# Performance work log

Hardware: AMD Instinct MI355X
Metric: run time of the kernel (lower is better)

The kernel has to match this reference:

```python
import jax, jax.numpy as jnp
import numpy as np

EPS = 1e-5

def _bn(x, g, b):
    # training-mode batchnorm over all axes except the last (channel)
    axes = tuple(range(x.ndim - 1))
    m = x.mean(axis=axes, keepdims=True)
    v = x.var(axis=axes, keepdims=True)
    return (x - m) * jax.lax.rsqrt(v + EPS) * g + b

def setup_inputs() -> dict:
    key = jax.random.key(0)
    ks = jax.random.split(key, 9)
    B, N = 4, 4096
    def w(i, shape, fan_in):
        return jax.random.normal(ks[i], shape, jnp.float32) * np.float32(1.0 / np.sqrt(fan_in))
    return {
        "x": jax.random.normal(ks[0], (B, 3, N), jnp.float32),
        "Wq": w(1, (64, 3), 3),
        "Wkv": w(2, (128, 3), 3),
        "Wp1": w(3, (64, 3), 3),
        "Wp2": w(4, (64, 64), 64),
        "Wa": w(5, (64, 64), 64),
        "Wc1": w(6, (64, 64), 64),
        "Wsk": w(7, (64, 6), 6),
        "Wga": w(8, (64, 128), 128),
        "g_p": jnp.ones(64, jnp.float32), "b_p": jnp.zeros(64, jnp.float32),
        "g_a": jnp.ones(64, jnp.float32), "b_a": jnp.zeros(64, jnp.float32),
        "g_c": jnp.ones(64, jnp.float32), "b_c": jnp.zeros(64, jnp.float32),
        "g_sk": jnp.ones(64, jnp.float32), "b_sk": jnp.zeros(64, jnp.float32),
        "g_ga": jnp.ones(64, jnp.float32), "b_ga": jnp.zeros(64, jnp.float32),
        "k": 32,
    }

def reference(x, Wq, Wkv, Wp1, Wp2, Wa, Wc1, Wsk, Wga,
              g_p, b_p, g_a, b_a, g_c, b_c, g_sk, b_sk, g_ga, b_ga, k):
    # x: [B, 3, N] point cloud
    xt = jnp.transpose(x, (0, 2, 1))                      # [B, N, 3]
    B = xt.shape[0]
    # --- KNN neighbor grouping (irregular gather) ---
    sq = jnp.sum(xt * xt, axis=-1)                        # [B, N]
    dist = sq[:, :, None] + sq[:, None, :] - 2.0 * jnp.einsum('bnc,bmc->bnm', xt, xt)
    _, idx = jax.lax.top_k(-dist, k)                      # [B, N, k]
    grouped = xt[jnp.arange(B)[:, None, None], idx]       # [B, N, k, 3]
    rel = grouped - xt[:, :, None, :]                     # relative coords
    # --- local self-attention (1x1 conv QKV + position encoding) ---
    q = jnp.einsum('bnc,dc->bnd', xt, Wq)[:, :, None, :]  # [B, N, 1, 64]
    kv = jnp.einsum('bnkc,dc->bnkd', rel, Wkv)            # [B, N, k, 128]
    kf, vf = kv[..., :64], kv[..., 64:]
    pos = jnp.einsum('bnkd,ed->bnke',
                     jax.nn.relu(_bn(jnp.einsum('bnkc,dc->bnkd', rel, Wp1), g_p, b_p)),
                     Wp2)                                 # [B, N, k, 64]
    logits = jax.nn.relu(_bn(jnp.einsum('bnkd,ed->bnke', q - kf + pos, Wa), g_a, b_a))
    attn = jax.nn.softmax(logits, axis=2)                 # softmax over k neighbors
    agg = jnp.sum(attn * (vf + pos), axis=2)              # [B, N, 64]
    # --- pointnet conv-BN head + skip + fusion ---
    h = jax.nn.relu(_bn(jnp.einsum('bnd,ed->bne', agg, Wc1), g_c, b_c))
    nb_max = jnp.max(grouped, axis=2)                     # [B, N, 3] max-pool over neighbors
    sk = jax.nn.relu(_bn(jnp.einsum('bnc,dc->bnd',
                                    jnp.concatenate([xt, nb_max], axis=-1), Wsk), g_sk, b_sk))
    out = jax.nn.relu(_bn(jnp.einsum('bnc,dc->bnd',
                                     jnp.concatenate([h, sk], axis=-1), Wga), g_ga, b_ga))
    return jnp.transpose(out, (0, 2, 1))                  # [B, 64, N]
```

## Files before the change

### kernel.cpp

```cpp
#include <hip/hip_runtime.h>

#define NBATCH 4
#define NPTS   4096
#define NP     (NBATCH*NPTS)
#define KK     32
#define INF    __builtin_inff()

static const size_t OFF_PTS  = 0;
static const size_t OFF_IDX  = 65536;
static const size_t OFF_TSK  = 589824;
static const size_t OFF_TC   = 1638400;
static const size_t OFF_TGA  = 2686976;
static const size_t OFF_PREL = 3735552;
static const size_t OFF_PSK  = 3735568;
static const size_t OFF_PTA  = 3735696;
static const size_t OFF_PTC  = 3735824;
static const size_t OFF_PTGA = 3735952;
static const size_t OFF_AFF  = 3736080;

typedef __bf16 bf16x8  __attribute__((ext_vector_type(8)));
typedef float  floatx16 __attribute__((ext_vector_type(16)));
#define MFMA32(a,b,c) __builtin_amdgcn_mfma_f32_32x32x16_bf16(a, b, c, 0, 0, 0)

union F8 { bf16x8 v; unsigned short us[8]; uint4 q4; };

__device__ __forceinline__ unsigned short bfbits(float f) {
  unsigned u = __float_as_uint(f);
  return (unsigned short)((u + 0x7FFFu + ((u >> 16) & 1u)) >> 16);
}
__device__ __forceinline__ floatx16 zero16() {
  floatx16 v;
#pragma unroll
  for (int i = 0; i < 16; ++i) v[i] = 0.f;
  return v;
}
__device__ __forceinline__ float wsum(float v) {
#pragma unroll
  for (int o = 32; o; o >>= 1) v += __shfl_xor(v, o, 64);
  return v;
}

__global__ __launch_bounds__(256,1) void k_prep(const float* __restrict__ x, float4* __restrict__ pts,
                                                float* __restrict__ pta, float* __restrict__ ptc,
                                                float* __restrict__ ptga, float* __restrict__ prel9,
                                                float* __restrict__ psk128) {
  if (blockIdx.x == 0) {
    if (threadIdx.x < 128) {
      pta[threadIdx.x] = 0.f; ptc[threadIdx.x] = 0.f; ptga[threadIdx.x] = 0.f;
      psk128[threadIdx.x] = 0.f;
    }
    if (threadIdx.x < 16) prel9[threadIdx.x] = 0.f;
  }
  int g = blockIdx.x * 256 + threadIdx.x;
  int b = g / NPTS, n = g % NPTS;
  float vx = x[(b*3+0)*NPTS + n];
  float vy = x[(b*3+1)*NPTS + n];
  float vz = x[(b*3+2)*NPTS + n];
  pts[g] = make_float4(vx, vy, vz, vx*vx + vy*vy + vz*vz);
}

__global__ __launch_bounds__(256) void k_knn(const float4* __restrict__ pts, int* __restrict__ idx,
                                             const float* __restrict__ Wsk, float* __restrict__ tsk,
                                             float* __restrict__ prel9, float* __restrict__ psk128) {
  __shared__ __align__(16) float4 tile[1024];
  __shared__ int ocnt[4];
  __shared__ int lsel[128];
  __shared__ float rsum[9], psum[64], pss[64];
  const int tid  = threadIdx.x;
  const int w    = tid >> 6;
  const int lane = tid & 63;
  if (tid < 9)  rsum[tid] = 0.f;
  if (tid < 64) { psum[tid] = 0.f; pss[tid] = 0.f; }
  const int n = blockIdx.x * 4 + w;
  const int batch = n >> 12;
  const float4* base = pts + batch * NPTS;
  const float4 me = pts[n];
  const float wk0 = Wsk[lane*6+0], wk1 = Wsk[lane*6+1], wk2 = Wsk[lane*6+2],
              wk3 = Wsk[lane*6+3], wk4 = Wsk[lane*6+4], wk5 = Wsk[lane*6+5];

  unsigned keys[64];
  unsigned t0 = 0xFFFFFFFFu, t1 = 0xFFFFFFFFu, t2 = 0xFFFFFFFFu, t3 = 0xFFFFFFFFu;
  for (int st = 0; st < 4; ++st) {
    __syncthreads();
#pragma unroll
    for (int r = 0; r < 4; ++r)
      tile[r*256 + tid] = base[st*1024 + r*256 + tid];
    __syncthreads();
#pragma unroll
    for (int j = 0; j < 16; ++j) {
      float4 p = tile[j*64 + lane];
      float dot = fmaf(me.x, p.x, fmaf(me.y, p.y, me.z * p.z));
      float d = fmaxf(fmaf(-2.f, dot, me.w + p.w), 0.f);
      unsigned k = __float_as_uint(d);
      keys[st*16 + j] = k;
      unsigned m = k, x;
      x = min(t0, m); m = max(t0, m); t0 = x;
      x = min(t1, m); m = max(t1, m); t1 = x;
      x = min(t2, m); m = max(t2, m); t2 = x;
      t3 = min(t3, m);
    }
  }

  unsigned glo = t0, ghi = t3;
#pragma unroll
  for (int o = 32; o; o >>= 1) {
    glo = min(glo, (unsigned)__shfl_xor((int)glo, o));
    ghi = max(ghi, (unsigned)__shfl_xor((int)ghi, o));
  }

  unsigned lo = glo, hi = ghi, tau = ghi;
  bool exact = false;
  while (lo < hi) {
    unsigned mid = lo + ((hi - lo) >> 1);
    int c = (t0 <= mid) + (t1 <= mid) + (t2 <= mid) + (t3 <= mid);
#pragma unroll
    for (int o = 32; o; o >>= 1) c += __shfl_xor(c, o);
    if (c == 32) { tau = mid; exact = true; break; }
    if (c > 32) hi = mid; else lo = mid + 1;
  }
  if (!exact) tau = lo;

  if (__ballot(t3 <= tau) != 0ull) {
    lo = glo; hi = tau; exact = false;
    while (lo < hi) {
      unsigned mid = lo + ((hi - lo) >> 1);
      int c = 0;
#pragma unroll
      for (int t = 0; t < 64; ++t) c += (keys[t] <= mid) ? 1 : 0;
#pragma unroll
      for (int o = 32; o; o >>= 1) c += __shfl_xor(c, o);
      if (c == 32) { tau = mid; exact = true; break; }
      if (c > 32) hi = mid; else lo = mid + 1;
    }
    if (!exact) tau = lo;
  }

  if (lane == 0) ocnt[w] = 0;
  int* op = idx + n * KK;
#pragma unroll
  for (int t = 0; t < 64; ++t) {
    bool take = exact ? (keys[t] <= tau) : (keys[t] < tau);
    if (take) {
      int s = atomicAdd(&ocnt[w], 1);
      int m = (t >> 4) * 1024 + (t & 15) * 64 + lane;
      op[s] = m; lsel[w*32 + s] = m;
    }
  }
  if (!exact) {
    unsigned long long em = 0;
#pragma unroll
    for (int t = 0; t < 64; ++t) if (keys[t] == tau) em |= 1ull << t;
    int n1 = ocnt[w];
    int need = 32 - n1;
    for (int f = 0; f < need; ++f) {
      int myt = em ? (int)__builtin_ctzll(em) : 64;
      int mym = (myt < 64) ? ((myt >> 4) * 1024 + (myt & 15) * 64 + lane) : 0x7FFFFFFF;
      int g = mym;
#pragma unroll
      for (int o = 32; o; o >>= 1) g = min(g, __shfl_xor(g, o));
      if (mym == g && myt < 64) { em &= em - 1; op[n1 + f] = mym; lsel[w*32 + n1 + f] = mym; }
    }
  }

  int mi = lsel[w*32 + (lane & 31)];
  float4 p = base[mi];
  bool act = lane < 32;
  float r0 = act ? p.x - me.x : 0.f;
  float r1 = act ? p.y - me.y : 0.f;
  float r2 = act ? p.z - me.z : 0.f;
  float vals[9] = { r0, r1, r2, r0*r0, r0*r1, r0*r2, r1*r1, r1*r2, r2*r2 };
#pragma unroll
  for (int t = 0; t < 9; ++t) {
    float rs = wsum(vals[t]);
    if (lane == 0) atomicAdd(&rsum[t], rs);
  }
  float nx = act ? p.x : -INF, ny = act ? p.y : -INF, nz = act ? p.z : -INF;
#pragma unroll
  for (int o = 32; o; o >>= 1) {
    nx = fmaxf(nx, __shfl_xor(nx, o));
    ny = fmaxf(ny, __shfl_xor(ny, o));
    nz = fmaxf(nz, __shfl_xor(nz, o));
  }
  float ts = fmaf(me.x, wk0, fmaf(me.y, wk1, fmaf(me.z, wk2,
             fmaf(nx, wk3, fmaf(ny, wk4, nz * wk5)))));
  tsk[n*64 + lane] = ts;
  atomicAdd(&psum[lane], ts);
  atomicAdd(&pss[lane], ts * ts);
  __syncthreads();
  if (tid < 9)  atomicAdd(&prel9[tid], rsum[tid]);
  if (tid < 64) atomicAdd(&psk128[tid], psum[tid]);
  else if (tid < 128) atomicAdd(&psk128[tid], pss[tid - 64]);
}

__global__ __launch_bounds__(64,1) void k_fin1(const float* __restrict__ prel9, const float* __restrict__ psk128,
                                               const float* __restrict__ Wp1,
                                               const float* __restrict__ g_p, const float* __restrict__ b_p,
                                               const float* __restrict__ g_sk, const float* __restrict__ b_sk,
                                               float* __restrict__ aff) {
  int d = threadIdx.x;
  double C = (double)NP * (double)KK;
  double mr0 = prel9[0]/C, mr1 = prel9[1]/C, mr2 = prel9[2]/C;
  double e00 = prel9[3]/C, e01 = prel9[4]/C, e02 = prel9[5]/C;
  double e11 = prel9[6]/C, e12 = prel9[7]/C, e22 = prel9[8]/C;
  double w0 = Wp1[d*3+0], w1 = Wp1[d*3+1], w2 = Wp1[d*3+2];
  double mu  = w0*mr0 + w1*mr1 + w2*mr2;
  double ex2 = w0*w0*e00 + w1*w1*e11 + w2*w2*e22 + 2.0*(w0*w1*e01 + w0*w2*e02 + w1*w2*e12);
  double var = ex2 - mu*mu;
  double sc  = (double)g_p[d] / sqrt(var + 1e-5);
  aff[0*64 + d] = (float)sc;
  aff[1*64 + d] = (float)((double)b_p[d] - mu*sc);
  double mean = (double)psk128[d] / (double)NP;
  double v2   = (double)psk128[64+d] / (double)NP - mean*mean;
  double sc4  = (double)g_sk[d] / sqrt(v2 + 1e-5);
  aff[6*64 + d] = (float)sc4;
  aff[7*64 + d] = (float)((double)b_sk[d] - mean*sc4);
}

__global__ __launch_bounds__(64,1) void k_fin2(const float* __restrict__ st, double C,
                                               const float* __restrict__ g, const float* __restrict__ b,
                                               float* __restrict__ s_out, float* __restrict__ o_out) {
  int d = threadIdx.x;
  double mean = (double)st[d] / C;
  double var  = (double)st[64 + d] / C - mean*mean;
  double sc   = (double)g[d] / sqrt(var + 1e-5);
  s_out[d] = (float)sc;
  o_out[d] = (float)((double)b[d] - mean*sc);
}

template<int MODE>
__global__ __launch_bounds__(256,1) void k_entry(const float4* __restrict__ pts, const int* __restrict__ idx,
                                                 const float* __restrict__ Wq, const float* __restrict__ Wkv,
                                                 const float* __restrict__ Wp1, const float* __restrict__ Wp2,
                                                 const float* __restrict__ Wa, const float* __restrict__ Wc1,
                                                 const float* __restrict__ aff, float* __restrict__ pstats,
                                                 float* __restrict__ tc) {
  __shared__ __align__(16) unsigned short ybuf[4][32][72];
  __shared__ __align__(16) float aggbuf[4][64];
  __shared__ float psum[64], pss[64];
  if (threadIdx.x < 64) { psum[threadIdx.x] = 0.f; pss[threadIdx.x] = 0.f; }
  __syncthreads();
  const int lane = threadIdx.x & 63;
  const int w    = threadIdx.x >> 6;
  const int c    = lane & 31;
  const int q5   = lane >> 5;

  F8 B0[2];
#pragma unroll
  for (int nt = 0; nt < 2; ++nt)
#pragma unroll
    for (int t = 0; t < 8; ++t)
      B0[nt].us[t] = (q5 == 0 && t < 3) ? bfbits(Wp1[(nt*32+c)*3 + t]) : (unsigned short)0;

  F8 Bs[4][2], B2[4][2];
#pragma unroll
  for (int kt = 0; kt < 4; ++kt)
#pragma unroll
    for (int h = 0; h < 2; ++h) {
      const float* p2 = Wp2 + (h*32+c)*64 + kt*16 + q5*8;
      float4 a = *(const float4*)p2, b = *(const float4*)(p2 + 4);
      Bs[kt][h].us[0]=bfbits(a.x); Bs[kt][h].us[1]=bfbits(a.y); Bs[kt][h].us[2]=bfbits(a.z); Bs[kt][h].us[3]=bfbits(a.w);
      Bs[kt][h].us[4]=bfbits(b.x); Bs[kt][h].us[5]=bfbits(b.y); Bs[kt][h].us[6]=bfbits(b.z); Bs[kt][h].us[7]=bfbits(b.w);
      const float* pa = Wa + (h*32+c)*64 + kt*16 + q5*8;
      float4 e = *(const float4*)pa, f = *(const float4*)(pa + 4);
      B2[kt][h].us[0]=bfbits(e.x); B2[kt][h].us[1]=bfbits(e.y); B2[kt][h].us[2]=bfbits(e.z); B2[kt][h].us[3]=bfbits(e.w);
      B2[kt][h].us[4]=bfbits(f.x); B2[kt][h].us[5]=bfbits(f.y); B2[kt][h].us[6]=bfbits(f.z); B2[kt][h].us[7]=bfbits(f.w);
    }

  F8 Bk4[4];
#pragma unroll
  for (int nt = 0; nt < 4; ++nt) {
    if (MODE == 0 && nt >= 2) { for (int t = 0; t < 8; ++t) Bk4[nt].us[t] = 0; continue; }
    int e = (nt & 1)*32 + c;
#pragma unroll
    for (int t = 0; t < 8; ++t)
      Bk4[nt].us[t] = (q5 == 0 && t < 3)
        ? bfbits(nt < 2 ? -Wkv[e*3 + t] : Wkv[(64+e)*3 + t]) : (unsigned short)0;
  }

  const float s1a = aff[c],      o1a = aff[64+c];
  const float s1b = aff[32+c],   o1b = aff[96+c];
  float s2a = 0.f, o2a = 0.f, s2b = 0.f, o2b = 0.f;
  if (MODE == 1) { s2a = aff[128+c]; o2a = aff[192+c]; s2b = aff[160+c]; o2b = aff[224+c]; }
  const float wqa0 = Wq[c*3+0],      wqa1 = Wq[c*3+1],      wqa2 = Wq[c*3+2];
  const float wqb0 = Wq[(32+c)*3+0], wqb1 = Wq[(32+c)*3+1], wqb2 = Wq[(32+c)*3+2];

  const int wave_id = blockIdx.x * 4 + w;
  const int n0 = wave_id * 8;
  const int batch = n0 >> 12;
  const float4* base = pts + batch * NPTS;

  for (int pi = 0; pi < 8; ++pi) {
    const int n = n0 + pi;
    const float4 me = pts[n];
    const int nb = idx[n*KK + c];
    const float4 pp = base[nb];
    const float r0 = pp.x - me.x, r1 = pp.y - me.y, r2 = pp.z - me.z;
    F8 relA;
#pragma unroll
    for (int t = 0; t < 8; ++t) relA.us[t] = 0;
    if (q5 == 0) { relA.us[0] = bfbits(r0); relA.us[1] = bfbits(r1); relA.us[2] = bfbits(r2); }

    const floatx16 z = zero16();
    floatx16 y0 = MFMA32(relA.v, B0[0].v, z);
    floatx16 y1 = MFMA32(relA.v, B0[1].v, z);
#pragma unroll
    for (int r = 0; r < 16; ++r) {
      int row = (r & 3) + 8*(r >> 2) + 4*q5;
      ybuf[w][row][c]      = bfbits(fmaxf(fmaf(y0[r], s1a, o1a), 0.f));
      ybuf[w][row][32 + c] = bfbits(fmaxf(fmaf(y1[r], s1b, o1b), 0.f));
    }
    F8 Ay[4];
#pragma unroll
    for (int kt = 0; kt < 4; ++kt) Ay[kt].q4 = *(const uint4*)&ybuf[w][c][kt*16 + q5*8];

    floatx16 Cp0 = z, Cp1 = z;
#pragma unroll
    for (int kt = 0; kt < 4; ++kt) {
      Cp0 = MFMA32(Ay[kt].v, Bs[kt][0].v, Cp0);
      Cp1 = MFMA32(Ay[kt].v, Bs[kt][1].v, Cp1);
    }
    floatx16 Cu0 = MFMA32(relA.v, Bk4[0].v, Cp0);
    floatx16 Cu1 = MFMA32(relA.v, Bk4[1].v, Cp1);
    if (MODE == 1) {
      Cp0 = MFMA32(relA.v, Bk4[2].v, Cp0);
      Cp1 = MFMA32(relA.v, Bk4[3].v, Cp1);
    }
    const float qa = fmaf(me.x, wqa0, fmaf(me.y, wqa1, me.z * wqa2));
    const float qb = fmaf(me.x, wqb0, fmaf(me.y, wqb1, me.z * wqb2));
#pragma unroll
    for (int r = 0; r < 16; ++r) {
      int row = (r & 3) + 8*(r >> 2) + 4*q5;
      ybuf[w][row][c]      = bfbits(Cu0[r] + qa);
      ybuf[w][row][32 + c] = bfbits(Cu1[r] + qb);
    }
    F8 Au[4];
#pragma unroll
    for (int kt = 0; kt < 4; ++kt) Au[kt].q4 = *(const uint4*)&ybuf[w][c][kt*16 + q5*8];
    floatx16 Ct0 = z, Ct1 = z;
#pragma unroll
    for (int kt = 0; kt < 4; ++kt) {
      Ct0 = MFMA32(Au[kt].v, B2[kt][0].v, Ct0);
      Ct1 = MFMA32(Au[kt].v, B2[kt][1].v, Ct1);
    }

    if (MODE == 0) {
      float sa = 0.f, qqa = 0.f, sb = 0.f, qqb = 0.f;
#pragma unroll
      for (int r = 0; r < 16; ++r) {
        sa += Ct0[r]; qqa = fmaf(Ct0[r], Ct0[r], qqa);
        sb += Ct1[r]; qqb = fmaf(Ct1[r], Ct1[r], qqb);
      }
      sa += __shfl_xor(sa, 32); qqa += __shfl_xor(qqa, 32);
      sb += __shfl_xor(sb, 32); qqb += __shfl_xor(qqb, 32);
      if (q5 == 0) {
        atomicAdd(&psum[c], sa);      atomicAdd(&pss[c], qqa);
        atomicAdd(&psum[32+c], sb);   atomicAdd(&pss[32+c], qqb);
      }
    } else {
      float ma = -INF, mb = -INF;
#pragma unroll
      for (int r = 0; r < 16; ++r) {
        float la = fmaxf(fmaf(Ct0[r], s2a, o2a), 0.f); Ct0[r] = la; ma = fmaxf(ma, la);
        float lb = fmaxf(fmaf(Ct1[r], s2b, o2b), 0.f); Ct1[r] = lb; mb = fmaxf(mb, lb);
      }
      ma = fmaxf(ma, __shfl_xor(ma, 32));
      mb = fmaxf(mb, __shfl_xor(mb, 32));
      float sa = 0.f, sb = 0.f, aga = 0.f, agb = 0.f;
#pragma unroll
      for (int r = 0; r < 16; ++r) {
        float ta = __expf(Ct0[r] - ma); sa += ta; aga = fmaf(ta, Cp0[r], aga);
        float tb = __expf(Ct1[r] - mb); sb += tb; agb = fmaf(tb, Cp1[r], agb);
      }
      sa += __shfl_xor(sa, 32); aga += __shfl_xor(aga, 32);
      sb += __shfl_xor(sb, 32); agb += __shfl_xor(agb, 32);
      if (q5 == 0) {
        aggbuf[w][c]      = aga / sa;
        aggbuf[w][32 + c] = agb / sb;
      }
      float acc = 0.f;
#pragma unroll
      for (int g = 0; g < 16; ++g) {
        float4 av = *(const float4*)&aggbuf[w][g*4];
        const float4 wv = *(const float4*)(Wc1 + lane*64 + g*4);
        acc = fmaf(av.x, wv.x, fmaf(av.y, wv.y, fmaf(av.z, wv.z, fmaf(av.w, wv.w, acc))));
      }
      tc[n*64 + lane] = acc;
      atomicAdd(&psum[lane], acc);
      atomicAdd(&pss[lane], acc * acc);
    }
  }
  __syncthreads();
  if (threadIdx.x < 64) atomicAdd(&pstats[threadIdx.x], psum[threadIdx.x]);
  else if (threadIdx.x < 128) atomicAdd(&pstats[threadIdx.x], pss[threadIdx.x - 64]);
}

__global__ __launch_bounds__(256,1) void k_final(const float* __restrict__ tcb, const float* __restrict__ tskb,
                                                 const float* __restrict__ Wga, const float* __restrict__ aff,
                                                 float* __restrict__ tga, float* __restrict__ pstats) {
  __shared__ __align__(16) float hb[4][64];
  __shared__ __align__(16) float sb[4][64];
  __shared__ float psum[64], pss[64];
  if (threadIdx.x < 64) { psum[threadIdx.x] = 0.f; pss[threadIdx.x] = 0.f; }
  __syncthreads();
  const int lane = threadIdx.x & 63;
  const int w    = threadIdx.x >> 6;
  const int n = blockIdx.x * 4 + w;
  hb[w][lane] = fmaxf(fmaf(tcb[n*64 + lane],  aff[256 + lane], aff[320 + lane]), 0.f);
  sb[w][lane] = fmaxf(fmaf(tskb[n*64 + lane], aff[384 + lane], aff[448 + lane]), 0.f);
  float g0=0,g1=0,g2=0,g3=0;
#pragma unroll
  for (int d = 0; d < 64; d += 4) {
    const float4 hv = *(const float4*)&hb[w][d];
    const float4 wg = *(const float4*)(Wga + lane*128 + d);
    g0 = fmaf(hv.x, wg.x, g0);
    g1 = fmaf(hv.y, wg.y, g1);
    g2 = fmaf(hv.z, wg.z, g2);
    g3 = fmaf(hv.w, wg.w, g3);
  }
#pragma unroll
  for (int d = 0; d < 64; d += 4) {
    const float4 sv = *(const float4*)&sb[w][d];
    const float4 wg = *(const float4*)(Wga + lane*128 + 64 + d);
    g0 = fmaf(sv.x, wg.x, g0);
    g1 = fmaf(sv.y, wg.y, g1);
    g2 = fmaf(sv.z, wg.z, g2);
    g3 = fmaf(sv.w, wg.w, g3);
  }
  const float tg = (g0+g1) + (g2+g3);
  tga[n*64 + lane] = tg;
  atomicAdd(&psum[lane], tg);
  atomicAdd(&pss[lane], tg * tg);
  __syncthreads();
  if (threadIdx.x < 64) atomicAdd(&pstats[threadIdx.x], psum[threadIdx.x]);
  else if (threadIdx.x < 128) atomicAdd(&pstats[threadIdx.x], pss[threadIdx.x - 64]);
}

__global__ __launch_bounds__(256,1) void k_out(const float* __restrict__ tga, const float* __restrict__ aff,
                                               float* __restrict__ out) {
  int g = blockIdx.x * 256 + threadIdx.x;
  int nn = g & 4095;
  int e  = (g >> 12) & 63;
  int b  = g >> 18;
  float v = tga[((b << 12) + nn) * 64 + e];
  out[g] = fmaxf(fmaf(v, aff[512 + e], aff[576 + e]), 0.f);
}

extern "C" void kernel_launch(void* const* d_in, const int* in_sizes, int n_in,
                              void* d_out, int out_size, void* d_ws, size_t ws_size,
                              hipStream_t stream) {
  const float* x    = (const float*)d_in[0];
  const float* Wq   = (const float*)d_in[1];
  const float* Wkv  = (const float*)d_in[2];
  const float* Wp1  = (const float*)d_in[3];
  const float* Wp2  = (const float*)d_in[4];
  const float* Wa   = (const float*)d_in[5];
  const float* Wc1  = (const float*)d_in[6];
  const float* Wsk  = (const float*)d_in[7];
  const float* Wga  = (const float*)d_in[8];
  const float* g_p  = (const float*)d_in[9];
  const float* b_p  = (const float*)d_in[10];
  const float* g_a  = (const float*)d_in[11];
  const float* b_a  = (const float*)d_in[12];
  const float* g_c  = (const float*)d_in[13];
  const float* b_c  = (const float*)d_in[14];
  const float* g_sk = (const float*)d_in[15];
  const float* b_sk = (const float*)d_in[16];
  const float* g_ga = (const float*)d_in[17];
  const float* b_ga = (const float*)d_in[18];
  float* W = (float*)d_ws;
  float4*  pts   = (float4*)(W + OFF_PTS);
  int*     idx   = (int*)(W + OFF_IDX);
  float*   tsk   = W + OFF_TSK;
  float*   tc    = W + OFF_TC;
  float*   tga   = W + OFF_TGA;
  float*   prel9 = W + OFF_PREL;
  float*   psk   = W + OFF_PSK;
  float*   pta   = W + OFF_PTA;
  float*   ptc   = W + OFF_PTC;
  float*   ptga  = W + OFF_PTGA;
  float*   aff   = W + OFF_AFF;
  float*   out   = (float*)d_out;

  k_prep<<<64, 256, 0, stream>>>(x, pts, pta, ptc, ptga, prel9, psk);
  k_knn<<<4096, 256, 0, stream>>>(pts, idx, Wsk, tsk, prel9, psk);
  k_fin1<<<1, 64, 0, stream>>>(prel9, psk, Wp1, g_p, b_p, g_sk, b_sk, aff);
  k_entry<0><<<512, 256, 0, stream>>>(pts, idx, Wq, Wkv, Wp1, Wp2, Wa, nullptr, aff, pta, nullptr);
  k_fin2<<<1, 64, 0, stream>>>(pta, (double)NP * (double)KK, g_a, b_a, aff + 128, aff + 192);
  k_entry<1><<<512, 256, 0, stream>>>(pts, idx, Wq, Wkv, Wp1, Wp2, Wa, Wc1, aff, ptc, tc);
  k_fin2<<<1, 64, 0, stream>>>(ptc, (double)NP, g_c, b_c, aff + 256, aff + 320);
  k_final<<<4096, 256, 0, stream>>>(tc, tsk, Wga, aff, tga, ptga);
  k_fin2<<<1, 64, 0, stream>>>(ptga, (double)NP, g_ga, b_ga, aff + 512, aff + 576);
  k_out<<<4096, 256, 0, stream>>>(tga, aff, out);
}
```

Baseline: 475.0 us.

## Drop per-lane key cache in KNN; recompute distances from global memory

The KNN kernel no longer keeps 64 distance keys per lane in registers or stages points through a shared-memory tile. Distances are recomputed straight from global (L2-resident) point data in each pass: the initial scan, the fallback bisection and the selection pass. Each lane now tracks a top-6 list instead of a top-4, which makes the expensive fallback bisection less likely. The goal is to cut register pressure and raise occupancy, at the cost of extra global loads and distance arithmetic, especially when the fallback path is taken.

```diff
diff --git a/kernel.cpp b/kernel.cpp
--- a/kernel.cpp
+++ b/kernel.cpp
@@ -39,6 +39,11 @@
   for (int o = 32; o; o >>= 1) v += __shfl_xor(v, o, 64);
   return v;
 }
+__device__ __forceinline__ int isum(int v) {
+#pragma unroll
+  for (int o = 32; o; o >>= 1) v += __shfl_xor(v, o);
+  return v;
+}
 
 __global__ __launch_bounds__(256,1) void k_prep(const float* __restrict__ x, float4* __restrict__ pts,
                                                 float* __restrict__ pta, float* __restrict__ ptc,
@@ -62,7 +67,6 @@
 __global__ __launch_bounds__(256) void k_knn(const float4* __restrict__ pts, int* __restrict__ idx,
                                              const float* __restrict__ Wsk, float* __restrict__ tsk,
                                              float* __restrict__ prel9, float* __restrict__ psk128) {
-  __shared__ __align__(16) float4 tile[1024];
   __shared__ int ocnt[4];
   __shared__ int lsel[128];
   __shared__ float rsum[9], psum[64], pss[64];
@@ -71,6 +75,7 @@
   const int lane = tid & 63;
   if (tid < 9)  rsum[tid] = 0.f;
   if (tid < 64) { psum[tid] = 0.f; pss[tid] = 0.f; }
+  __syncthreads();
   const int n = blockIdx.x * 4 + w;
   const int batch = n >> 12;
   const float4* base = pts + batch * NPTS;
@@ -78,30 +83,23 @@
   const float wk0 = Wsk[lane*6+0], wk1 = Wsk[lane*6+1], wk2 = Wsk[lane*6+2],
               wk3 = Wsk[lane*6+3], wk4 = Wsk[lane*6+4], wk5 = Wsk[lane*6+5];
 
-  unsigned keys[64];
-  unsigned t0 = 0xFFFFFFFFu, t1 = 0xFFFFFFFFu, t2 = 0xFFFFFFFFu, t3 = 0xFFFFFFFFu;
-  for (int st = 0; st < 4; ++st) {
-    __syncthreads();
-#pragma unroll
-    for (int r = 0; r < 4; ++r)
-      tile[r*256 + tid] = base[st*1024 + r*256 + tid];
-    __syncthreads();
-#pragma unroll
-    for (int j = 0; j < 16; ++j) {
-      float4 p = tile[j*64 + lane];
-      float dot = fmaf(me.x, p.x, fmaf(me.y, p.y, me.z * p.z));
-      float d = fmaxf(fmaf(-2.f, dot, me.w + p.w), 0.f);
-      unsigned k = __float_as_uint(d);
-      keys[st*16 + j] = k;
-      unsigned m = k, x;
-      x = min(t0, m); m = max(t0, m); t0 = x;
-      x = min(t1, m); m = max(t1, m); t1 = x;
-      x = min(t2, m); m = max(t2, m); t2 = x;
-      t3 = min(t3, m);
-    }
-  }
-
-  unsigned glo = t0, ghi = t3;
+  unsigned t0 = 0xFFFFFFFFu, t1 = 0xFFFFFFFFu, t2 = 0xFFFFFFFFu,
+           t3 = 0xFFFFFFFFu, t4 = 0xFFFFFFFFu, t5 = 0xFFFFFFFFu;
+#pragma unroll 4
+  for (int j = 0; j < 64; ++j) {
+    float4 p = base[j*64 + lane];
+    float dot = fmaf(me.x, p.x, fmaf(me.y, p.y, me.z * p.z));
+    float d = fmaxf(fmaf(-2.f, dot, me.w + p.w), 0.f);
+    unsigned m = __float_as_uint(d), x;
+    x = min(t0, m); m = max(t0, m); t0 = x;
+    x = min(t1, m); m = max(t1, m); t1 = x;
+    x = min(t2, m); m = max(t2, m); t2 = x;
+    x = min(t3, m); m = max(t3, m); t3 = x;
+    x = min(t4, m); m = max(t4, m); t4 = x;
+    t5 = min(t5, m);
+  }
+
+  unsigned glo = t0, ghi = t5;
 #pragma unroll
   for (int o = 32; o; o >>= 1) {
     glo = min(glo, (unsigned)__shfl_xor((int)glo, o));
@@ -112,23 +110,26 @@
   bool exact = false;
   while (lo < hi) {
     unsigned mid = lo + ((hi - lo) >> 1);
-    int c = (t0 <= mid) + (t1 <= mid) + (t2 <= mid) + (t3 <= mid);
-#pragma unroll
-    for (int o = 32; o; o >>= 1) c += __shfl_xor(c, o);
+    int c = (t0 <= mid) + (t1 <= mid) + (t2 <= mid) +
+            (t3 <= mid) + (t4 <= mid) + (t5 <= mid);
+    c = isum(c);
     if (c == 32) { tau = mid; exact = true; break; }
     if (c > 32) hi = mid; else lo = mid + 1;
   }
   if (!exact) tau = lo;
 
-  if (__ballot(t3 <= tau) != 0ull) {
+  if (__ballot(t5 <= tau) != 0ull) {
     lo = glo; hi = tau; exact = false;
     while (lo < hi) {
       unsigned mid = lo + ((hi - lo) >> 1);
       int c = 0;
-#pragma unroll
-      for (int t = 0; t < 64; ++t) c += (keys[t] <= mid) ? 1 : 0;
-#pragma unroll
-      for (int o = 32; o; o >>= 1) c += __shfl_xor(c, o);
+      for (int j = 0; j < 64; ++j) {
+        float4 p = base[j*64 + lane];
+        float dot = fmaf(me.x, p.x, fmaf(me.y, p.y, me.z * p.z));
+        float d = fmaxf(fmaf(-2.f, dot, me.w + p.w), 0.f);
+        c += (__float_as_uint(d) <= mid) ? 1 : 0;
+      }
+      c = isum(c);
       if (c == 32) { tau = mid; exact = true; break; }
       if (c > 32) hi = mid; else lo = mid + 1;
     }
@@ -137,28 +138,31 @@
 
   if (lane == 0) ocnt[w] = 0;
   int* op = idx + n * KK;
-#pragma unroll
-  for (int t = 0; t < 64; ++t) {
-    bool take = exact ? (keys[t] <= tau) : (keys[t] < tau);
+  unsigned long long em = 0;
+#pragma unroll 4
+  for (int j = 0; j < 64; ++j) {
+    float4 p = base[j*64 + lane];
+    float dot = fmaf(me.x, p.x, fmaf(me.y, p.y, me.z * p.z));
+    float d = fmaxf(fmaf(-2.f, dot, me.w + p.w), 0.f);
+    unsigned k = __float_as_uint(d);
+    bool take = exact ? (k <= tau) : (k < tau);
     if (take) {
       int s = atomicAdd(&ocnt[w], 1);
-      int m = (t >> 4) * 1024 + (t & 15) * 64 + lane;
-      op[s] = m; lsel[w*32 + s] = m;
-    }
+      int m = j*64 + lane;
+      if (s < KK) { op[s] = m; lsel[w*32 + s] = m; }
+    }
+    if (k == tau) em |= 1ull << j;
   }
   if (!exact) {
-    unsigned long long em = 0;
-#pragma unroll
-    for (int t = 0; t < 64; ++t) if (keys[t] == tau) em |= 1ull << t;
     int n1 = ocnt[w];
-    int need = 32 - n1;
+    int need = KK - n1;
     for (int f = 0; f < need; ++f) {
-      int myt = em ? (int)__builtin_ctzll(em) : 64;
-      int mym = (myt < 64) ? ((myt >> 4) * 1024 + (myt & 15) * 64 + lane) : 0x7FFFFFFF;
+      int myj = em ? (int)__builtin_ctzll(em) : 64;
+      int mym = (myj < 64) ? (myj*64 + lane) : 0x7FFFFFFF;
       int g = mym;
 #pragma unroll
       for (int o = 32; o; o >>= 1) g = min(g, __shfl_xor(g, o));
-      if (mym == g && myt < 64) { em &= em - 1; op[n1 + f] = mym; lsel[w*32 + n1 + f] = mym; }
+      if (mym == g && myj < 64) { em &= em - 1; op[n1 + f] = mym; lsel[w*32 + n1 + f] = mym; }
     }
   }
 
```

Result: slower. 489.0 us (+2.9%).
